# Kernel tuning notes

Measured on AMD Instinct MI355X. Metric: run time of the kernel, lower is better.

## Reference

```python
import jax, jax.numpy as jnp
import numpy as np

N_NODES = 50000
N_EDGES = 800000
N_GRAPHS = 64
IN_DIM, HID1, HID2, N_CLASSES = 128, 256, 128, 10


def setup_inputs() -> dict:
    key = jax.random.key(0)
    ks = jax.random.split(key, 12)
    x = jax.random.normal(ks[0], (N_NODES, IN_DIM), dtype=jnp.float32)
    src = jax.random.randint(ks[1], (N_EDGES,), 0, N_NODES, dtype=jnp.int32)
    dst = jax.random.randint(ks[2], (N_EDGES,), 0, N_NODES, dtype=jnp.int32)
    graph_id = jnp.sort(jax.random.randint(ks[3], (N_NODES,), 0, N_GRAPHS, dtype=jnp.int32))
    s1 = 1.0 / np.sqrt(IN_DIM)
    s2 = 1.0 / np.sqrt(HID1)
    s3 = 1.0 / np.sqrt(HID2)
    s4 = 1.0 / np.sqrt(12)
    return {
        'x': x, 'src': src, 'dst': dst, 'graph_id': graph_id,
        'W1': jax.random.normal(ks[4], (IN_DIM, HID1), dtype=jnp.float32) * s1,
        'b1': jnp.zeros((HID1,), dtype=jnp.float32),
        'W2': jax.random.normal(ks[5], (HID1, HID2), dtype=jnp.float32) * s2,
        'b2': jnp.zeros((HID2,), dtype=jnp.float32),
        'Wc1': jax.random.normal(ks[6], (HID2, 12), dtype=jnp.float32) * s3,
        'bc1': jnp.zeros((12,), dtype=jnp.float32),
        'Wc2': jax.random.normal(ks[7], (12, 12), dtype=jnp.float32) * s4,
        'bc2': jnp.zeros((12,), dtype=jnp.float32),
        'Wc3': jax.random.normal(ks[8], (12, N_CLASSES), dtype=jnp.float32) * s4,
        'bc3': jnp.zeros((N_CLASSES,), dtype=jnp.float32),
    }


def _graph_conv(x, W, b, src, dst, inv_sqrt_out, inv_sqrt_in, n_nodes):
    # DGL GraphConv, norm='both': D_out^{-1/2} applied to source feats,
    # sum-aggregate over edges, then D_in^{-1/2} on destination, then +bias.
    # Weight applied first (equivalent by linearity; reduces gather traffic
    # when out_dim < in_dim, and is exactly what DGL does in that case).
    xw = (x * inv_sqrt_out[:, None]) @ W                      # [N, out]
    agg = jax.ops.segment_sum(xw[src], dst, num_segments=n_nodes)  # SpMM
    return agg * inv_sqrt_in[:, None] + b


def reference(x, src, dst, graph_id, W1, b1, W2, b2, Wc1, bc1, Wc2, bc2, Wc3, bc3):
    n = x.shape[0]
    ones_e = jnp.ones(src.shape, dtype=x.dtype)
    deg_out = jnp.maximum(jax.ops.segment_sum(ones_e, src, num_segments=n), 1.0)
    deg_in = jnp.maximum(jax.ops.segment_sum(ones_e, dst, num_segments=n), 1.0)
    inv_o = jax.lax.rsqrt(deg_out)
    inv_i = jax.lax.rsqrt(deg_in)

    h = jax.nn.relu(_graph_conv(x, W1, b1, src, dst, inv_o, inv_i, n))
    h = jax.nn.relu(_graph_conv(h, W2, b2, src, dst, inv_o, inv_i, n))

    # dgl.mean_nodes: per-graph mean over nodes of the batched graph
    gsum = jax.ops.segment_sum(h, graph_id, num_segments=N_GRAPHS)   # [G, HID2]
    cnt = jnp.maximum(jax.ops.segment_sum(jnp.ones((n,), dtype=h.dtype), graph_id, num_segments=N_GRAPHS), 1.0)
    hg = gsum / cnt[:, None]

    # tiny 3-layer MLP (no activations in between, as in the source)
    out = hg @ Wc1 + bc1
    out = out @ Wc2 + bc2
    out = out @ Wc3 + bc3
    return out
```

## Files before the change

### kernel.cpp

```cpp
#include <hip/hip_runtime.h>
#include <hip/hip_bf16.h>

#define IN_DIM 128
#define HID1 256
#define HID2 128
#define QS_INV (6.0f / 127.0f)
#define QS_FWD (127.0f / 6.0f)

#define HB_BINS 12500
#define HB_WORDS 6250
#define HB_CHUNKS 64
#define BK_SHIFT 8
#define NBUCK 196
#define NCHUNK 256
#define PADCAP 2048

__global__ __launch_bounds__(256) void hist_coarse(const int* __restrict__ src,
                                                   const int* __restrict__ dst, int E,
                                                   int hchunk, int schunk, int nhist,
                                                   int* __restrict__ part, int N,
                                                   int* __restrict__ ccnt,
                                                   float* __restrict__ hg, int hg_n) {
    __shared__ int sm[HB_WORDS];
    __shared__ int cnt[NBUCK];
    const int b = blockIdx.x;
    const int t = threadIdx.x;
    if (b < nhist) {
        const int base = (b >> 6) * HB_BINS;
        const int ebeg = (b & 63) * hchunk;
        const int eend = min(ebeg + hchunk, E);
        for (int w = t; w < HB_WORDS; w += 256) sm[w] = 0;
        __syncthreads();
        for (int e = ebeg + t; e < eend; e += 256) {
            int v = src[e] - base;
            if ((unsigned)v < (unsigned)HB_BINS)
                atomicAdd(&sm[v >> 1], 1 << ((v & 1) * 16));
        }
        __syncthreads();
        const int nb = min(HB_BINS, N - base);
        int* dp = part + (size_t)(b & 63) * N + base;
        for (int w = t; 2 * w < nb; w += 256) {
            int packed = sm[w];
            int bb = 2 * w;
            dp[bb] = packed & 0xffff;
            if (bb + 1 < nb) dp[bb + 1] = (packed >> 16) & 0xffff;
        }
    } else {
        const int cid = b - nhist;
        if (cid == 0)
            for (int i = t; i < hg_n; i += 256) hg[i] = 0.f;
        for (int i = t; i < NBUCK; i += 256) cnt[i] = 0;
        __syncthreads();
        int ebeg = cid * schunk, eend = min(ebeg + schunk, E);
        for (int e = ebeg + t; e < eend; e += 256)
            atomicAdd(&cnt[dst[e] >> BK_SHIFT], 1);
        __syncthreads();
        for (int i = t; i < NBUCK; i += 256) ccnt[cid * NBUCK + i] = cnt[i];
    }
}

__global__ __launch_bounds__(NCHUNK) void coarse_col(const int* __restrict__ ccnt,
                                                     int* __restrict__ coffpre,
                                                     int* __restrict__ ctot) {
    __shared__ int sm[NCHUNK];
    const int b = blockIdx.x, t = threadIdx.x;
    int v = ccnt[t * NBUCK + b];
    sm[t] = v;
    __syncthreads();
#pragma unroll
    for (int off = 1; off < NCHUNK; off <<= 1) {
        int u = (t >= off) ? sm[t - off] : 0;
        __syncthreads();
        sm[t] += u;
        __syncthreads();
    }
    coffpre[t * NBUCK + b] = sm[t] - v;
    if (t == NCHUNK - 1) ctot[b] = sm[t];
}

__device__ __forceinline__ void scan_bbase(const int* __restrict__ ctot, int* sm, int* bbase) {
    const int t = threadIdx.x;
    int v = (t < NBUCK) ? ctot[t] : 0;
    sm[t] = v;
    __syncthreads();
#pragma unroll
    for (int off = 1; off < 256; off <<= 1) {
        int u = (t >= off) ? sm[t - off] : 0;
        __syncthreads();
        sm[t] += u;
        __syncthreads();
    }
    if (t < NBUCK) bbase[t] = sm[t] - v;
    __syncthreads();
}

__global__ __launch_bounds__(256) void scat_cvt(const int* __restrict__ src,
                                                const int* __restrict__ dst, int E,
                                                int schunk,
                                                const int* __restrict__ coffpre,
                                                const int* __restrict__ ctot,
                                                int2* __restrict__ pairs,
                                                const float* __restrict__ x,
                                                const int* __restrict__ part,
                                                float* __restrict__ inv_o,
                                                float* __restrict__ w_arr,
                                                unsigned char* __restrict__ x_q,
                                                __hip_bfloat16* __restrict__ xw2_bf, int N,
                                                int nNodeBlk,
                                                const float* __restrict__ W1,
                                                __hip_bfloat16* __restrict__ W1t,
                                                const float* __restrict__ W2,
                                                __hip_bfloat16* __restrict__ W2t) {
    const int S1 = IN_DIM * HID1;
    const int S2 = HID1 * HID2;
    __shared__ int sm[256];
    __shared__ int bbase[NBUCK];
    __shared__ int lcur[NBUCK];
    const int b = blockIdx.x;
    const int t = threadIdx.x;
    if (b < NCHUNK) {
        scan_bbase(ctot, sm, bbase);
        for (int i = t; i < NBUCK; i += 256)
            lcur[i] = bbase[i] + coffpre[b * NBUCK + i];
        __syncthreads();
        int ebeg = b * schunk, eend = min(ebeg + schunk, E);
        for (int e = ebeg + t; e < eend; e += 256) {
            int d = dst[e];
            int p = atomicAdd(&lcur[d >> BK_SHIFT], 1);
            pairs[p] = make_int2(src[e], d);
        }
    } else if (b < NCHUNK + nNodeBlk) {
        const int n0 = (b - NCHUNK) * 256;
        const int node = n0 + t;
        if (node < N) {
            int d = 0;
#pragma unroll 4
            for (int ch = 0; ch < HB_CHUNKS; ++ch) d += part[(size_t)ch * N + node];
            float iv = rsqrtf((float)max(d, 1));
            inv_o[node] = iv;
            w_arr[node] = iv * QS_INV;
        }
#pragma unroll 4
        for (int k = 0; k < 32; ++k) {
            int li = k * 256 + t;
            int nl = li >> 5;
            if (n0 + nl < N) {
                int i = n0 * 32 + li;
                float4 v = reinterpret_cast<const float4*>(x)[i];
                int c0 = __float2int_rn(fminf(fmaxf(v.x * QS_FWD, -127.f), 127.f));
                int c1 = __float2int_rn(fminf(fmaxf(v.y * QS_FWD, -127.f), 127.f));
                int c2 = __float2int_rn(fminf(fmaxf(v.z * QS_FWD, -127.f), 127.f));
                int c3 = __float2int_rn(fminf(fmaxf(v.w * QS_FWD, -127.f), 127.f));
                unsigned int pk = (unsigned int)(c0 & 0xff) | ((unsigned int)(c1 & 0xff) << 8) |
                                  ((unsigned int)(c2 & 0xff) << 16) | ((unsigned int)(c3 & 0xff) << 24);
                reinterpret_cast<unsigned int*>(x_q)[i] = pk;
            }
        }
    } else if (b < NCHUNK + nNodeBlk + 256) {
        int idx = (b - NCHUNK - nNodeBlk) * 256 + t;
        if (idx < S1) {
            int k = idx / HID1, n = idx - k * HID1;
            W1t[n * IN_DIM + k] = __float2bfloat16(W1[idx]);
        } else if (idx < S1 + S2) {
            int j = idx - S1;
            int k = j / HID2, n = j - k * HID2;
            W2t[n * HID1 + k] = __float2bfloat16(W2[j]);
        }
    } else {
        if (t < 32)
            reinterpret_cast<unsigned int*>(x_q)[(size_t)N * 32 + t] = 0u;
        else if (t < 64)
            reinterpret_cast<ushort4*>(xw2_bf)[(size_t)N * 32 + (t - 32)] = make_ushort4(0, 0, 0, 0);
    }
}

__global__ __launch_bounds__(256) void scat_b(const int2* __restrict__ pairs,
                                              const int* __restrict__ ctot, int N,
                                              const float* __restrict__ w_arr,
                                              int* __restrict__ rowb,
                                              int* __restrict__ rowe,
                                              float* __restrict__ inv_i,
                                              int* __restrict__ csr_src) {
    __shared__ int sm[256];
    __shared__ int bbase[NBUCK];
    __shared__ int cnt[1 << BK_SHIFT];
    __shared__ int cur[1 << BK_SHIFT];
    const int b = blockIdx.x, t = threadIdx.x;
    scan_bbase(ctot, sm, bbase);
    const int segBase = bbase[b];
    const int segEnd = segBase + ctot[b];
    const int pSegBase = ((bbase[b] + 7) & ~7) + b * PADCAP;
    const int nb0 = b << BK_SHIFT;
    const int nbn = min(256, N - nb0);
    cnt[t] = 0;
    __syncthreads();
    for (int j = segBase + t; j < segEnd; j += 256)
        atomicAdd(&cnt[pairs[j].y - nb0], 1);
    __syncthreads();
    int v = cnt[t];
    int pv = (v + 7) & ~7;
    sm[t] = pv;
    __syncthreads();
#pragma unroll
    for (int off = 1; off < 256; off <<= 1) {
        int u = (t >= off) ? sm[t - off] : 0;
        __syncthreads();
        sm[t] += u;
        __syncthreads();
    }
    int pexcl = sm[t] - pv;
    int pbeg = pSegBase + pexcl;
    cur[t] = pbeg;
    if (t < nbn) {
        rowb[nb0 + t] = pbeg;
        rowe[nb0 + t] = pbeg + pv;
        inv_i[nb0 + t] = rsqrtf((float)max(v, 1));
        for (int k = v; k < pv; ++k) csr_src[pbeg + k] = N;
    }
    __syncthreads();
    for (int j = segBase + t; j < segEnd; j += 256) {
        int2 pr = pairs[j];
        int p = atomicAdd(&cur[pr.y - nb0], 1);
        __hip_bfloat16 wb = __float2bfloat16(w_arr[pr.x]);
        csr_src[p] = ((int)(*(unsigned short*)&wb) << 16) | pr.x;
    }
}

__device__ __forceinline__ void gather_row_i8(const unsigned short* __restrict__ xq,
                                              const int* __restrict__ csr,
                                              int beg, int end, int lane,
                                              float& A0, float& A1) {
    float a0 = 0.f, a1 = 0.f;
    int j = beg;
    for (; j + 16 <= end; j += 16) {
        int4 e0 = *reinterpret_cast<const int4*>(csr + j);
        int4 e1 = *reinterpret_cast<const int4*>(csr + j + 4);
        int4 e2 = *reinterpret_cast<const int4*>(csr + j + 8);
        int4 e3 = *reinterpret_cast<const int4*>(csr + j + 12);
        unsigned short q0  = xq[(size_t)(e0.x & 0xffff) * 64 + lane];
        unsigned short q1  = xq[(size_t)(e0.y & 0xffff) * 64 + lane];
        unsigned short q2  = xq[(size_t)(e0.z & 0xffff) * 64 + lane];
        unsigned short q3  = xq[(size_t)(e0.w & 0xffff) * 64 + lane];
        unsigned short q4  = xq[(size_t)(e1.x & 0xffff) * 64 + lane];
        unsigned short q5  = xq[(size_t)(e1.y & 0xffff) * 64 + lane];
        unsigned short q6  = xq[(size_t)(e1.z & 0xffff) * 64 + lane];
        unsigned short q7  = xq[(size_t)(e1.w & 0xffff) * 64 + lane];
        unsigned short q8  = xq[(size_t)(e2.x & 0xffff) * 64 + lane];
        unsigned short q9  = xq[(size_t)(e2.y & 0xffff) * 64 + lane];
        unsigned short q10 = xq[(size_t)(e2.z & 0xffff) * 64 + lane];
        unsigned short q11 = xq[(size_t)(e2.w & 0xffff) * 64 + lane];
        unsigned short q12 = xq[(size_t)(e3.x & 0xffff) * 64 + lane];
        unsigned short q13 = xq[(size_t)(e3.y & 0xffff) * 64 + lane];
        unsigned short q14 = xq[(size_t)(e3.z & 0xffff) * 64 + lane];
        unsigned short q15 = xq[(size_t)(e3.w & 0xffff) * 64 + lane];
#define ACC_I8(ev, qv) { \
        float w = __uint_as_float((unsigned int)(ev) & 0xffff0000u); \
        a0 += w * (float)(int)(signed char)((qv) & 0xff); \
        a1 += w * (float)(int)(signed char)((qv) >> 8); }
        ACC_I8(e0.x, q0)  ACC_I8(e0.y, q1)  ACC_I8(e0.z, q2)  ACC_I8(e0.w, q3)
        ACC_I8(e1.x, q4)  ACC_I8(e1.y, q5)  ACC_I8(e1.z, q6)  ACC_I8(e1.w, q7)
        ACC_I8(e2.x, q8)  ACC_I8(e2.y, q9)  ACC_I8(e2.z, q10) ACC_I8(e2.w, q11)
        ACC_I8(e3.x, q12) ACC_I8(e3.y, q13) ACC_I8(e3.z, q14) ACC_I8(e3.w, q15)
    }
    if (j + 8 <= end) {
        int4 e0 = *reinterpret_cast<const int4*>(csr + j);
        int4 e1 = *reinterpret_cast<const int4*>(csr + j + 4);
        unsigned short q0 = xq[(size_t)(e0.x & 0xffff) * 64 + lane];
        unsigned short q1 = xq[(size_t)(e0.y & 0xffff) * 64 + lane];
        unsigned short q2 = xq[(size_t)(e0.z & 0xffff) * 64 + lane];
        unsigned short q3 = xq[(size_t)(e0.w & 0xffff) * 64 + lane];
        unsigned short q4 = xq[(size_t)(e1.x & 0xffff) * 64 + lane];
        unsigned short q5 = xq[(size_t)(e1.y & 0xffff) * 64 + lane];
        unsigned short q6 = xq[(size_t)(e1.z & 0xffff) * 64 + lane];
        unsigned short q7 = xq[(size_t)(e1.w & 0xffff) * 64 + lane];
        ACC_I8(e0.x, q0) ACC_I8(e0.y, q1) ACC_I8(e0.z, q2) ACC_I8(e0.w, q3)
        ACC_I8(e1.x, q4) ACC_I8(e1.y, q5) ACC_I8(e1.z, q6) ACC_I8(e1.w, q7)
        j += 8;
    }
    for (; j < end; ++j) {
        int ev = csr[j];
        unsigned short qv = xq[(size_t)(ev & 0xffff) * 64 + lane];
        ACC_I8(ev, qv)
    }
#undef ACC_I8
    A0 = a0; A1 = a1;
}

__global__ __launch_bounds__(256) void spmm_kernel(const unsigned short* __restrict__ xq,
                                                   const int* __restrict__ rowb,
                                                   const int* __restrict__ rowe,
                                                   const int* __restrict__ csr_src,
                                                   __hip_bfloat16* __restrict__ out_bf, int N) {
    const int node = blockIdx.x * 4 + (threadIdx.x >> 6);
    if (node >= N) return;
    const int lane = threadIdx.x & 63;
    float a0, a1;
    gather_row_i8(xq, csr_src, rowb[node], rowe[node], lane, a0, a1);
    __hip_bfloat16 b0 = __float2bfloat16(a0);
    __hip_bfloat16 b1 = __float2bfloat16(a1);
    unsigned int packed = (unsigned int)(*(unsigned short*)&b0) |
                          ((unsigned int)(*(unsigned short*)&b1) << 16);
    ((unsigned int*)out_bf)[(size_t)node * 64 + lane] = packed;
}

__device__ __forceinline__ void bf2_unpack(unsigned int p, float& lo, float& hi) {
    lo = __uint_as_float(p << 16);
    hi = __uint_as_float(p & 0xffff0000u);
}

__device__ __forceinline__ void gather_row(const unsigned int* __restrict__ fp,
                                           const int* __restrict__ csr_src,
                                           int beg, int end, int lane,
                                           float& A0, float& A1) {
    float a0 = 0.f, a1 = 0.f;
    int j = beg;
    for (; j + 16 <= end; j += 16) {
        int4 i0 = *reinterpret_cast<const int4*>(csr_src + j);
        int4 i1 = *reinterpret_cast<const int4*>(csr_src + j + 4);
        int4 i2 = *reinterpret_cast<const int4*>(csr_src + j + 8);
        int4 i3 = *reinterpret_cast<const int4*>(csr_src + j + 12);
        unsigned int p0  = fp[(size_t)(i0.x & 0xffff) * 64 + lane];
        unsigned int p1  = fp[(size_t)(i0.y & 0xffff) * 64 + lane];
        unsigned int p2  = fp[(size_t)(i0.z & 0xffff) * 64 + lane];
        unsigned int p3  = fp[(size_t)(i0.w & 0xffff) * 64 + lane];
        unsigned int p4  = fp[(size_t)(i1.x & 0xffff) * 64 + lane];
        unsigned int p5  = fp[(size_t)(i1.y & 0xffff) * 64 + lane];
        unsigned int p6  = fp[(size_t)(i1.z & 0xffff) * 64 + lane];
        unsigned int p7  = fp[(size_t)(i1.w & 0xffff) * 64 + lane];
        unsigned int p8  = fp[(size_t)(i2.x & 0xffff) * 64 + lane];
        unsigned int p9  = fp[(size_t)(i2.y & 0xffff) * 64 + lane];
        unsigned int p10 = fp[(size_t)(i2.z & 0xffff) * 64 + lane];
        unsigned int p11 = fp[(size_t)(i2.w & 0xffff) * 64 + lane];
        unsigned int p12 = fp[(size_t)(i3.x & 0xffff) * 64 + lane];
        unsigned int p13 = fp[(size_t)(i3.y & 0xffff) * 64 + lane];
        unsigned int p14 = fp[(size_t)(i3.z & 0xffff) * 64 + lane];
        unsigned int p15 = fp[(size_t)(i3.w & 0xffff) * 64 + lane];
        float lo, hi;
        bf2_unpack(p0,  lo, hi); a0 += lo; a1 += hi;
        bf2_unpack(p1,  lo, hi); a0 += lo; a1 += hi;
        bf2_unpack(p2,  lo, hi); a0 += lo; a1 += hi;
        bf2_unpack(p3,  lo, hi); a0 += lo; a1 += hi;
        bf2_unpack(p4,  lo, hi); a0 += lo; a1 += hi;
        bf2_unpack(p5,  lo, hi); a0 += lo; a1 += hi;
        bf2_unpack(p6,  lo, hi); a0 += lo; a1 += hi;
        bf2_unpack(p7,  lo, hi); a0 += lo; a1 += hi;
        bf2_unpack(p8,  lo, hi); a0 += lo; a1 += hi;
        bf2_unpack(p9,  lo, hi); a0 += lo; a1 += hi;
        bf2_unpack(p10, lo, hi); a0 += lo; a1 += hi;
        bf2_unpack(p11, lo, hi); a0 += lo; a1 += hi;
        bf2_unpack(p12, lo, hi); a0 += lo; a1 += hi;
        bf2_unpack(p13, lo, hi); a0 += lo; a1 += hi;
        bf2_unpack(p14, lo, hi); a0 += lo; a1 += hi;
        bf2_unpack(p15, lo, hi); a0 += lo; a1 += hi;
    }
    if (j + 8 <= end) {
        int4 i0 = *reinterpret_cast<const int4*>(csr_src + j);
        int4 i1 = *reinterpret_cast<const int4*>(csr_src + j + 4);
        unsigned int p0 = fp[(size_t)(i0.x & 0xffff) * 64 + lane];
        unsigned int p1 = fp[(size_t)(i0.y & 0xffff) * 64 + lane];
        unsigned int p2 = fp[(size_t)(i0.z & 0xffff) * 64 + lane];
        unsigned int p3 = fp[(size_t)(i0.w & 0xffff) * 64 + lane];
        unsigned int p4 = fp[(size_t)(i1.x & 0xffff) * 64 + lane];
        unsigned int p5 = fp[(size_t)(i1.y & 0xffff) * 64 + lane];
        unsigned int p6 = fp[(size_t)(i1.z & 0xffff) * 64 + lane];
        unsigned int p7 = fp[(size_t)(i1.w & 0xffff) * 64 + lane];
        float lo, hi;
        bf2_unpack(p0, lo, hi); a0 += lo; a1 += hi;
        bf2_unpack(p1, lo, hi); a0 += lo; a1 += hi;
        bf2_unpack(p2, lo, hi); a0 += lo; a1 += hi;
        bf2_unpack(p3, lo, hi); a0 += lo; a1 += hi;
        bf2_unpack(p4, lo, hi); a0 += lo; a1 += hi;
        bf2_unpack(p5, lo, hi); a0 += lo; a1 += hi;
        bf2_unpack(p6, lo, hi); a0 += lo; a1 += hi;
        bf2_unpack(p7, lo, hi); a0 += lo; a1 += hi;
        j += 8;
    }
    for (; j < end; ++j) {
        unsigned int p0 = fp[(size_t)(csr_src[j] & 0xffff) * 64 + lane];
        float lo, hi;
        bf2_unpack(p0, lo, hi); a0 += lo; a1 += hi;
    }
    A0 = a0; A1 = a1;
}

#define SP_NODES 8
__global__ __launch_bounds__(256) void spmm_pool_kernel(const __hip_bfloat16* __restrict__ feat,
                                                        const int* __restrict__ rowb,
                                                        const int* __restrict__ rowe,
                                                        const int* __restrict__ csr_src,
                                                        const float* __restrict__ inv_i,
                                                        const float* __restrict__ b2,
                                                        const int* __restrict__ graph_id,
                                                        int N, float* __restrict__ hg_sum) {
    const int wave = blockIdx.x * 4 + (threadIdx.x >> 6);
    const int lane = threadIdx.x & 63;
    const int n0 = wave * SP_NODES;
    if (n0 >= N) return;
    const int n1 = min(n0 + SP_NODES, N);
    const unsigned int* fp = (const unsigned int*)feat;
    const float bias0 = b2[2 * lane];
    const float bias1 = b2[2 * lane + 1];
    int g = graph_id[n0];
    float p0s = 0.f, p1s = 0.f;
    for (int node = n0; node < n1; ++node) {
        int gi = graph_id[node];
        if (gi != g) {
            atomicAdd(&hg_sum[g * HID2 + 2 * lane], p0s);
            atomicAdd(&hg_sum[g * HID2 + 2 * lane + 1], p1s);
            p0s = p1s = 0.f;
            g = gi;
        }
        float a0, a1;
        gather_row(fp, csr_src, rowb[node], rowe[node], lane, a0, a1);
        float ii = inv_i[node];
        p0s += fmaxf(a0 * ii + bias0, 0.f);
        p1s += fmaxf(a1 * ii + bias1, 0.f);
    }
    atomicAdd(&hg_sum[g * HID2 + 2 * lane], p0s);
    atomicAdd(&hg_sum[g * HID2 + 2 * lane + 1], p1s);
}

#define GBM 128
#define GBN 128
#define GBK 32
typedef __attribute__((ext_vector_type(4))) float floatx4;
typedef __attribute__((ext_vector_type(8))) short shortx8;

__device__ __forceinline__ void gload_lds16(const void* g, void* l) {
    __builtin_amdgcn_global_load_lds(
        (const __attribute__((address_space(1))) unsigned int*)g,
        (__attribute__((address_space(3))) unsigned int*)l, 16, 0, 0);
}

__global__ __launch_bounds__(256) void mfma_gemm_kernel(const __hip_bfloat16* __restrict__ A,
                                                        const __hip_bfloat16* __restrict__ Bt,
                                                        __hip_bfloat16* __restrict__ C,
                                                        const float* __restrict__ scaleR,
                                                        const float* __restrict__ bias,
                                                        const float* __restrict__ scaleO,
                                                        int M, int Nn, int K, int doRelu) {
    __shared__ __align__(16) __hip_bfloat16 As[GBM * GBK];
    __shared__ __align__(16) __hip_bfloat16 Bs[GBN * GBK];
    const int tid = threadIdx.x;
    const int bm = blockIdx.x * GBM;
    const int bn = blockIdx.y * GBN;
    const int wid = tid >> 6;
    const int lane = tid & 63;
    const int wm = (wid & 1) * 64;
    const int wn = (wid >> 1) * 64;
    const int lrow = lane & 15;
    const int quad = lane >> 4;

    floatx4 acc[4][4] = {};

    for (int k0 = 0; k0 < K; k0 += GBK) {
#pragma unroll
        for (int c = 0; c < 2; ++c) {
            int slot = c * 256 + tid;
            int r = slot >> 2;
            int ko = (slot & 3) << 3;
            gload_lds16(A + (size_t)(bm + r) * K + k0 + ko,
                        (char*)As + c * 4096 + wid * 1024);
        }
#pragma unroll
        for (int c = 0; c < 2; ++c) {
            int slot = c * 256 + tid;
            int r = slot >> 2;
            int ko = (slot & 3) << 3;
            gload_lds16(Bt + (size_t)(bn + r) * K + k0 + ko,
                        (char*)Bs + c * 4096 + wid * 1024);
        }
        __syncthreads();

        shortx8 af[4], bf[4];
#pragma unroll
        for (int i = 0; i < 4; ++i)
            af[i] = *reinterpret_cast<const shortx8*>(&As[(wm + i * 16 + lrow) * GBK + quad * 8]);
#pragma unroll
        for (int i = 0; i < 4; ++i)
            bf[i] = *reinterpret_cast<const shortx8*>(&Bs[(wn + i * 16 + lrow) * GBK + quad * 8]);
#pragma unroll
        for (int im = 0; im < 4; ++im)
#pragma unroll
            for (int in = 0; in < 4; ++in)
                acc[im][in] = __builtin_amdgcn_mfma_f32_16x16x32_bf16(af[im], bf[in], acc[im][in], 0, 0, 0);
        __syncthreads();
    }

    float bv[4];
#pragma unroll
    for (int in = 0; in < 4; ++in)
        bv[in] = bias ? bias[bn + wn + in * 16 + lrow] : 0.f;

#pragma unroll
    for (int im = 0; im < 4; ++im) {
#pragma unroll
        for (int reg = 0; reg < 4; ++reg) {
            int r = bm + wm + im * 16 + quad * 4 + reg;
            if (r >= M) continue;
            float sR = scaleR ? scaleR[r] : 1.f;
            float sO = scaleO ? scaleO[r] : 1.f;
#pragma unroll
            for (int in = 0; in < 4; ++in) {
                int cc = bn + wn + in * 16 + lrow;
                float v = acc[im][in][reg] * sR + bv[in];
                if (doRelu) v = fmaxf(v, 0.f);
                v *= sO;
                C[(size_t)r * Nn + cc] = __float2bfloat16(v);
            }
        }
    }
}

__device__ __forceinline__ int lower_bound_i(const int* a, int n, int key) {
    int lo = 0, hi = n;
    while (lo < hi) {
        int mid = (lo + hi) >> 1;
        if (a[mid] < key) lo = mid + 1; else hi = mid;
    }
    return lo;
}

__global__ __launch_bounds__(64) void mlp_kernel(const float* __restrict__ hg_sum,
                                                 const int* __restrict__ graph_id, int n,
                                                 const float* __restrict__ Wc1, const float* __restrict__ bc1,
                                                 const float* __restrict__ Wc2, const float* __restrict__ bc2,
                                                 const float* __restrict__ Wc3, const float* __restrict__ bc3,
                                                 float* __restrict__ out) {
    const int g = blockIdx.x;
    const int t = threadIdx.x;
    __shared__ float h[HID2];
    __shared__ float t1[12];
    __shared__ float t2[12];
    __shared__ float s_inv_cnt;
    if (t == 0) {
        int beg = lower_bound_i(graph_id, n, g);
        int end = lower_bound_i(graph_id, n, g + 1);
        int c = end - beg;
        s_inv_cnt = 1.0f / (float)max(c, 1);
    }
    __syncthreads();
    const float ic = s_inv_cnt;
    for (int i = t; i < HID2; i += 64) h[i] = hg_sum[g * HID2 + i] * ic;
    __syncthreads();
    if (t < 12) {
        float a = bc1[t];
        for (int k = 0; k < HID2; ++k) a += h[k] * Wc1[k * 12 + t];
        t1[t] = a;
    }
    __syncthreads();
    if (t < 12) {
        float a = bc2[t];
        for (int k = 0; k < 12; ++k) a += t1[k] * Wc2[k * 12 + t];
        t2[t] = a;
    }
    __syncthreads();
    if (t < 10) {
        float a = bc3[t];
        for (int k = 0; k < 12; ++k) a += t2[k] * Wc3[k * 10 + t];
        out[g * 10 + t] = a;
    }
}

extern "C" void kernel_launch(void* const* d_in, const int* in_sizes, int n_in,
                              void* d_out, int out_size, void* d_ws, size_t ws_size,
                              hipStream_t stream) {
    const float* x        = (const float*)d_in[0];
    const int*   src      = (const int*)d_in[1];
    const int*   dst      = (const int*)d_in[2];
    const int*   graph_id = (const int*)d_in[3];
    const float* W1       = (const float*)d_in[4];
    const float* b1       = (const float*)d_in[5];
    const float* W2       = (const float*)d_in[6];
    const float* b2       = (const float*)d_in[7];
    const float* Wc1      = (const float*)d_in[8];
    const float* bc1      = (const float*)d_in[9];
    const float* Wc2      = (const float*)d_in[10];
    const float* bc2      = (const float*)d_in[11];
    const float* Wc3      = (const float*)d_in[12];
    const float* bc3      = (const float*)d_in[13];
    float* out = (float*)d_out;

    const int N = in_sizes[0] / IN_DIM;
    const int E = in_sizes[1];
    const int G = out_size / 10;

    char* ws = (char*)d_ws;
    size_t off = 0;
    auto alloc = [&](size_t bytes) -> char* {
        char* p = ws + off;
        off = (off + bytes + 255) & ~(size_t)255;
        return p;
    };
    float* inv_i   = (float*)alloc((size_t)N * 4);
    float* inv_o   = (float*)alloc((size_t)N * 4);
    float* w_arr   = (float*)alloc((size_t)N * 4);
    int*   rowb    = (int*)alloc((size_t)N * 4);
    int*   rowe    = (int*)alloc((size_t)N * 4);
    int*   ccnt    = (int*)alloc((size_t)NCHUNK * NBUCK * 4);
    int*   coffpre = (int*)alloc((size_t)NCHUNK * NBUCK * 4);
    int*   ctot    = (int*)alloc((size_t)NBUCK * 4);
    int2*  pairs   = (int2*)alloc((size_t)E * 8);
    int*   csr_src = (int*)alloc(((size_t)E + (size_t)NBUCK * PADCAP + 64) * 4);
    float* hg      = (float*)alloc((size_t)G * HID2 * 4);
    unsigned char* x_q = (unsigned char*)alloc((size_t)(N + 1) * IN_DIM);
    __hip_bfloat16* W1t     = (__hip_bfloat16*)alloc((size_t)IN_DIM * HID1 * 2);
    __hip_bfloat16* W2t     = (__hip_bfloat16*)alloc((size_t)HID1 * HID2 * 2);
    __hip_bfloat16* agg1_bf = (__hip_bfloat16*)alloc((size_t)N * IN_DIM * 2);
    __hip_bfloat16* h1_bf   = (__hip_bfloat16*)alloc((size_t)N * HID1 * 2);
    __hip_bfloat16* xw2_bf  = (__hip_bfloat16*)alloc((size_t)(N + 1) * HID2 * 2);

    int* part = (int*)h1_bf;

    const int hchunk = (E + HB_CHUNKS - 1) / HB_CHUNKS;
    const int n_ranges = (N + HB_BINS - 1) / HB_BINS;
    const int nhist = HB_CHUNKS * n_ranges;
    const int schunk = (E + NCHUNK - 1) / NCHUNK;
    hist_coarse<<<nhist + NCHUNK, 256, 0, stream>>>(src, dst, E, hchunk, schunk, nhist,
                                                    part, N, ccnt, hg, G * HID2);

    coarse_col<<<NBUCK, NCHUNK, 0, stream>>>(ccnt, coffpre, ctot);

    const int nNodeBlk = (N + 255) / 256;
    const int wblk = (IN_DIM * HID1 + HID1 * HID2 + 255) / 256;
    scat_cvt<<<NCHUNK + nNodeBlk + wblk + 1, 256, 0, stream>>>(
        src, dst, E, schunk, coffpre, ctot, pairs,
        x, part, inv_o, w_arr, x_q, xw2_bf, N, nNodeBlk, W1, W1t, W2, W2t);

    scat_b<<<NBUCK, 256, 0, stream>>>(pairs, ctot, N, w_arr, rowb, rowe, inv_i, csr_src);

    spmm_kernel<<<(N + 3) / 4, 256, 0, stream>>>((const unsigned short*)x_q, rowb, rowe,
                                                 csr_src, agg1_bf, N);
    mfma_gemm_kernel<<<dim3((N + GBM - 1) / GBM, HID1 / GBN), 256, 0, stream>>>(
        agg1_bf, W1t, h1_bf, inv_i, b1, inv_o, N, HID1, IN_DIM, 1);

    mfma_gemm_kernel<<<dim3((N + GBM - 1) / GBM, HID2 / GBN), 256, 0, stream>>>(
        h1_bf, W2t, xw2_bf, nullptr, nullptr, nullptr, N, HID2, HID1, 0);
    const int npw = (N + SP_NODES - 1) / SP_NODES;
    spmm_pool_kernel<<<(npw + 3) / 4, 256, 0, stream>>>(xw2_bf, rowb, rowe, csr_src, inv_i, b2,
                                                        graph_id, N, hg);

    mlp_kernel<<<G, 64, 0, stream>>>(hg, graph_id, N, Wc1, bc1, Wc2, bc2, Wc3, bc3, out);
}
```

Before: 255.1 us.

## Quantize layer-2 features to int8 with dynamic absmax before pooled SpMM gather

The second GEMM now computes a global absolute maximum of its bf16 output through a wave reduction and an atomicMax. A new kernel then quantizes xw2 to int8 using that scale, and the fused SpMM+pool kernel gathers 2-byte int8 pairs with integer accumulation instead of 4-byte bf16 pairs, rescaling once per node. This halves the random-gather traffic of the second aggregation. In exchange it adds an extra pass over xw2, an atomic reduction in the GEMM epilogue, and int8 quantization error.

Result: slower. 280.7 us (+10.0%).

```diff
diff --git a/kernel.cpp b/kernel.cpp
--- a/kernel.cpp
+++ b/kernel.cpp
@@ -20,7 +20,8 @@
                                                    int hchunk, int schunk, int nhist,
                                                    int* __restrict__ part, int N,
                                                    int* __restrict__ ccnt,
-                                                   float* __restrict__ hg, int hg_n) {
+                                                   float* __restrict__ hg, int hg_n,
+                                                   float* __restrict__ absm) {
     __shared__ int sm[HB_WORDS];
     __shared__ int cnt[NBUCK];
     const int b = blockIdx.x;
@@ -47,8 +48,10 @@
         }
     } else {
         const int cid = b - nhist;
-        if (cid == 0)
+        if (cid == 0) {
             for (int i = t; i < hg_n; i += 256) hg[i] = 0.f;
+            if (t == 0) *absm = 0.f;
+        }
         for (int i = t; i < NBUCK; i += 256) cnt[i] = 0;
         __syncthreads();
         int ebeg = cid * schunk, eend = min(ebeg + schunk, E);
@@ -303,88 +306,85 @@
     ((unsigned int*)out_bf)[(size_t)node * 64 + lane] = packed;
 }
 
-__device__ __forceinline__ void bf2_unpack(unsigned int p, float& lo, float& hi) {
-    lo = __uint_as_float(p << 16);
-    hi = __uint_as_float(p & 0xffff0000u);
-}
-
-__device__ __forceinline__ void gather_row(const unsigned int* __restrict__ fp,
-                                           const int* __restrict__ csr_src,
-                                           int beg, int end, int lane,
-                                           float& A0, float& A1) {
-    float a0 = 0.f, a1 = 0.f;
+__global__ __launch_bounds__(256) void quant2(const __hip_bfloat16* __restrict__ xw2,
+                                              const float* __restrict__ absm,
+                                              unsigned char* __restrict__ x2q, int n4) {
+    int i = blockIdx.x * 256 + threadIdx.x;
+    if (i >= n4) return;
+    float s = 127.f / fmaxf(*absm, 1e-20f);
+    uint2 v = reinterpret_cast<const uint2*>(xw2)[i];
+    float f0 = __uint_as_float(v.x << 16);
+    float f1 = __uint_as_float(v.x & 0xffff0000u);
+    float f2 = __uint_as_float(v.y << 16);
+    float f3 = __uint_as_float(v.y & 0xffff0000u);
+    int c0 = __float2int_rn(fminf(fmaxf(f0 * s, -127.f), 127.f));
+    int c1 = __float2int_rn(fminf(fmaxf(f1 * s, -127.f), 127.f));
+    int c2 = __float2int_rn(fminf(fmaxf(f2 * s, -127.f), 127.f));
+    int c3 = __float2int_rn(fminf(fmaxf(f3 * s, -127.f), 127.f));
+    unsigned int pk = (unsigned int)(c0 & 0xff) | ((unsigned int)(c1 & 0xff) << 8) |
+                      ((unsigned int)(c2 & 0xff) << 16) | ((unsigned int)(c3 & 0xff) << 24);
+    reinterpret_cast<unsigned int*>(x2q)[i] = pk;
+}
+
+__device__ __forceinline__ void gather_i8_sum(const unsigned short* __restrict__ xq,
+                                              const int* __restrict__ csr,
+                                              int beg, int end, int lane,
+                                              int& A0, int& A1) {
+    int a0 = 0, a1 = 0;
     int j = beg;
     for (; j + 16 <= end; j += 16) {
-        int4 i0 = *reinterpret_cast<const int4*>(csr_src + j);
-        int4 i1 = *reinterpret_cast<const int4*>(csr_src + j + 4);
-        int4 i2 = *reinterpret_cast<const int4*>(csr_src + j + 8);
-        int4 i3 = *reinterpret_cast<const int4*>(csr_src + j + 12);
-        unsigned int p0  = fp[(size_t)(i0.x & 0xffff) * 64 + lane];
-        unsigned int p1  = fp[(size_t)(i0.y & 0xffff) * 64 + lane];
-        unsigned int p2  = fp[(size_t)(i0.z & 0xffff) * 64 + lane];
-        unsigned int p3  = fp[(size_t)(i0.w & 0xffff) * 64 + lane];
-        unsigned int p4  = fp[(size_t)(i1.x & 0xffff) * 64 + lane];
-        unsigned int p5  = fp[(size_t)(i1.y & 0xffff) * 64 + lane];
-        unsigned int p6  = fp[(size_t)(i1.z & 0xffff) * 64 + lane];
-        unsigned int p7  = fp[(size_t)(i1.w & 0xffff) * 64 + lane];
-        unsigned int p8  = fp[(size_t)(i2.x & 0xffff) * 64 + lane];
-        unsigned int p9  = fp[(size_t)(i2.y & 0xffff) * 64 + lane];
-        unsigned int p10 = fp[(size_t)(i2.z & 0xffff) * 64 + lane];
-        unsigned int p11 = fp[(size_t)(i2.w & 0xffff) * 64 + lane];
-        unsigned int p12 = fp[(size_t)(i3.x & 0xffff) * 64 + lane];
-        unsigned int p13 = fp[(size_t)(i3.y & 0xffff) * 64 + lane];
-        unsigned int p14 = fp[(size_t)(i3.z & 0xffff) * 64 + lane];
-        unsigned int p15 = fp[(size_t)(i3.w & 0xffff) * 64 + lane];
-        float lo, hi;
-        bf2_unpack(p0,  lo, hi); a0 += lo; a1 += hi;
-        bf2_unpack(p1,  lo, hi); a0 += lo; a1 += hi;
-        bf2_unpack(p2,  lo, hi); a0 += lo; a1 += hi;
-        bf2_unpack(p3,  lo, hi); a0 += lo; a1 += hi;
-        bf2_unpack(p4,  lo, hi); a0 += lo; a1 += hi;
-        bf2_unpack(p5,  lo, hi); a0 += lo; a1 += hi;
-        bf2_unpack(p6,  lo, hi); a0 += lo; a1 += hi;
-        bf2_unpack(p7,  lo, hi); a0 += lo; a1 += hi;
-        bf2_unpack(p8,  lo, hi); a0 += lo; a1 += hi;
-        bf2_unpack(p9,  lo, hi); a0 += lo; a1 += hi;
-        bf2_unpack(p10, lo, hi); a0 += lo; a1 += hi;
-        bf2_unpack(p11, lo, hi); a0 += lo; a1 += hi;
-        bf2_unpack(p12, lo, hi); a0 += lo; a1 += hi;
-        bf2_unpack(p13, lo, hi); a0 += lo; a1 += hi;
-        bf2_unpack(p14, lo, hi); a0 += lo; a1 += hi;
-        bf2_unpack(p15, lo, hi); a0 += lo; a1 += hi;
+        int4 e0 = *reinterpret_cast<const int4*>(csr + j);
+        int4 e1 = *reinterpret_cast<const int4*>(csr + j + 4);
+        int4 e2 = *reinterpret_cast<const int4*>(csr + j + 8);
+        int4 e3 = *reinterpret_cast<const int4*>(csr + j + 12);
+        unsigned short q0  = xq[(size_t)(e0.x & 0xffff) * 64 + lane];
+        unsigned short q1  = xq[(size_t)(e0.y & 0xffff) * 64 + lane];
+        unsigned short q2  = xq[(size_t)(e0.z & 0xffff) * 64 + lane];
+        unsigned short q3  = xq[(size_t)(e0.w & 0xffff) * 64 + lane];
+        unsigned short q4  = xq[(size_t)(e1.x & 0xffff) * 64 + lane];
+        unsigned short q5  = xq[(size_t)(e1.y & 0xffff) * 64 + lane];
+        unsigned short q6  = xq[(size_t)(e1.z & 0xffff) * 64 + lane];
+        unsigned short q7  = xq[(size_t)(e1.w & 0xffff) * 64 + lane];
+        unsigned short q8  = xq[(size_t)(e2.x & 0xffff) * 64 + lane];
+        unsigned short q9  = xq[(size_t)(e2.y & 0xffff) * 64 + lane];
+        unsigned short q10 = xq[(size_t)(e2.z & 0xffff) * 64 + lane];
+        unsigned short q11 = xq[(size_t)(e2.w & 0xffff) * 64 + lane];
+        unsigned short q12 = xq[(size_t)(e3.x & 0xffff) * 64 + lane];
+        unsigned short q13 = xq[(size_t)(e3.y & 0xffff) * 64 + lane];
+        unsigned short q14 = xq[(size_t)(e3.z & 0xffff) * 64 + lane];
+        unsigned short q15 = xq[(size_t)(e3.w & 0xffff) * 64 + lane];
+#define ACC_S(qv) { a0 += (int)(signed char)((qv) & 0xff); a1 += (int)(signed char)((qv) >> 8); }
+        ACC_S(q0)  ACC_S(q1)  ACC_S(q2)  ACC_S(q3)
+        ACC_S(q4)  ACC_S(q5)  ACC_S(q6)  ACC_S(q7)
+        ACC_S(q8)  ACC_S(q9)  ACC_S(q10) ACC_S(q11)
+        ACC_S(q12) ACC_S(q13) ACC_S(q14) ACC_S(q15)
     }
     if (j + 8 <= end) {
-        int4 i0 = *reinterpret_cast<const int4*>(csr_src + j);
-        int4 i1 = *reinterpret_cast<const int4*>(csr_src + j + 4);
-        unsigned int p0 = fp[(size_t)(i0.x & 0xffff) * 64 + lane];
-        unsigned int p1 = fp[(size_t)(i0.y & 0xffff) * 64 + lane];
-        unsigned int p2 = fp[(size_t)(i0.z & 0xffff) * 64 + lane];
-        unsigned int p3 = fp[(size_t)(i0.w & 0xffff) * 64 + lane];
-        unsigned int p4 = fp[(size_t)(i1.x & 0xffff) * 64 + lane];
-        unsigned int p5 = fp[(size_t)(i1.y & 0xffff) * 64 + lane];
-        unsigned int p6 = fp[(size_t)(i1.z & 0xffff) * 64 + lane];
-        unsigned int p7 = fp[(size_t)(i1.w & 0xffff) * 64 + lane];
-        float lo, hi;
-        bf2_unpack(p0, lo, hi); a0 += lo; a1 += hi;
-        bf2_unpack(p1, lo, hi); a0 += lo; a1 += hi;
-        bf2_unpack(p2, lo, hi); a0 += lo; a1 += hi;
-        bf2_unpack(p3, lo, hi); a0 += lo; a1 += hi;
-        bf2_unpack(p4, lo, hi); a0 += lo; a1 += hi;
-        bf2_unpack(p5, lo, hi); a0 += lo; a1 += hi;
-        bf2_unpack(p6, lo, hi); a0 += lo; a1 += hi;
-        bf2_unpack(p7, lo, hi); a0 += lo; a1 += hi;
+        int4 e0 = *reinterpret_cast<const int4*>(csr + j);
+        int4 e1 = *reinterpret_cast<const int4*>(csr + j + 4);
+        unsigned short q0 = xq[(size_t)(e0.x & 0xffff) * 64 + lane];
+        unsigned short q1 = xq[(size_t)(e0.y & 0xffff) * 64 + lane];
+        unsigned short q2 = xq[(size_t)(e0.z & 0xffff) * 64 + lane];
+        unsigned short q3 = xq[(size_t)(e0.w & 0xffff) * 64 + lane];
+        unsigned short q4 = xq[(size_t)(e1.x & 0xffff) * 64 + lane];
+        unsigned short q5 = xq[(size_t)(e1.y & 0xffff) * 64 + lane];
+        unsigned short q6 = xq[(size_t)(e1.z & 0xffff) * 64 + lane];
+        unsigned short q7 = xq[(size_t)(e1.w & 0xffff) * 64 + lane];
+        ACC_S(q0) ACC_S(q1) ACC_S(q2) ACC_S(q3)
+        ACC_S(q4) ACC_S(q5) ACC_S(q6) ACC_S(q7)
         j += 8;
     }
     for (; j < end; ++j) {
-        unsigned int p0 = fp[(size_t)(csr_src[j] & 0xffff) * 64 + lane];
-        float lo, hi;
-        bf2_unpack(p0, lo, hi); a0 += lo; a1 += hi;
-    }
+        unsigned short qv = xq[(size_t)(csr[j] & 0xffff) * 64 + lane];
+        ACC_S(qv)
+    }
+#undef ACC_S
     A0 = a0; A1 = a1;
 }
 
 #define SP_NODES 8
-__global__ __launch_bounds__(256) void spmm_pool_kernel(const __hip_bfloat16* __restrict__ feat,
+__global__ __launch_bounds__(256) void spmm_pool_kernel(const unsigned short* __restrict__ x2q,
+                                                        const float* __restrict__ absm,
                                                         const int* __restrict__ rowb,
                                                         const int* __restrict__ rowe,
                                                         const int* __restrict__ csr_src,
@@ -397,7 +397,7 @@
     const int n0 = wave * SP_NODES;
     if (n0 >= N) return;
     const int n1 = min(n0 + SP_NODES, N);
-    const unsigned int* fp = (const unsigned int*)feat;
+    const float step = fmaxf(*absm, 1e-20f) * (1.0f / 127.0f);
     const float bias0 = b2[2 * lane];
     const float bias1 = b2[2 * lane + 1];
     int g = graph_id[n0];
@@ -410,11 +410,11 @@
             p0s = p1s = 0.f;
             g = gi;
         }
-        float a0, a1;
-        gather_row(fp, csr_src, rowb[node], rowe[node], lane, a0, a1);
-        float ii = inv_i[node];
-        p0s += fmaxf(a0 * ii + bias0, 0.f);
-        p1s += fmaxf(a1 * ii + bias1, 0.f);
+        int a0i, a1i;
+        gather_i8_sum(x2q, csr_src, rowb[node], rowe[node], lane, a0i, a1i);
+        float iis = inv_i[node] * step;
+        p0s += fmaxf((float)a0i * iis + bias0, 0.f);
+        p1s += fmaxf((float)a1i * iis + bias1, 0.f);
     }
     atomicAdd(&hg_sum[g * HID2 + 2 * lane], p0s);
     atomicAdd(&hg_sum[g * HID2 + 2 * lane + 1], p1s);
@@ -438,6 +438,7 @@
                                                         const float* __restrict__ scaleR,
                                                         const float* __restrict__ bias,
                                                         const float* __restrict__ scaleO,
+                                                        float* __restrict__ absmax_out,
                                                         int M, int Nn, int K, int doRelu) {
     __shared__ __align__(16) __hip_bfloat16 As[GBM * GBK];
     __shared__ __align__(16) __hip_bfloat16 Bs[GBN * GBK];
@@ -492,6 +493,7 @@
     for (int in = 0; in < 4; ++in)
         bv[in] = bias ? bias[bn + wn + in * 16 + lrow] : 0.f;
 
+    float mloc = 0.f;
 #pragma unroll
     for (int im = 0; im < 4; ++im) {
 #pragma unroll
@@ -506,9 +508,17 @@
                 float v = acc[im][in][reg] * sR + bv[in];
                 if (doRelu) v = fmaxf(v, 0.f);
                 v *= sO;
+                mloc = fmaxf(mloc, fabsf(v));
                 C[(size_t)r * Nn + cc] = __float2bfloat16(v);
             }
         }
+    }
+    if (absmax_out) {
+#pragma unroll
+        for (int off = 1; off < 64; off <<= 1)
+            mloc = fmaxf(mloc, __shfl_xor(mloc, off));
+        if (lane == 0)
+            atomicMax((unsigned int*)absmax_out, __float_as_uint(mloc));
     }
 }
 
@@ -595,6 +605,7 @@
     float* inv_i   = (float*)alloc((size_t)N * 4);
     float* inv_o   = (float*)alloc((size_t)N * 4);
     float* w_arr   = (float*)alloc((size_t)N * 4);
+    float* absm    = (float*)alloc(4);
     int*   rowb    = (int*)alloc((size_t)N * 4);
     int*   rowe    = (int*)alloc((size_t)N * 4);
     int*   ccnt    = (int*)alloc((size_t)NCHUNK * NBUCK * 4);
@@ -603,7 +614,8 @@
     int2*  pairs   = (int2*)alloc((size_t)E * 8);
     int*   csr_src = (int*)alloc(((size_t)E + (size_t)NBUCK * PADCAP + 64) * 4);
     float* hg      = (float*)alloc((size_t)G * HID2 * 4);
-    unsigned char* x_q = (unsigned char*)alloc((size_t)(N + 1) * IN_DIM);
+    unsigned char* x_q  = (unsigned char*)alloc((size_t)(N + 1) * IN_DIM);
+    unsigned char* x2q  = (unsigned char*)alloc((size_t)(N + 1) * HID2);
     __hip_bfloat16* W1t     = (__hip_bfloat16*)alloc((size_t)IN_DIM * HID1 * 2);
     __hip_bfloat16* W2t     = (__hip_bfloat16*)alloc((size_t)HID1 * HID2 * 2);
     __hip_bfloat16* agg1_bf = (__hip_bfloat16*)alloc((size_t)N * IN_DIM * 2);
@@ -617,7 +629,7 @@
     const int nhist = HB_CHUNKS * n_ranges;
     const int schunk = (E + NCHUNK - 1) / NCHUNK;
     hist_coarse<<<nhist + NCHUNK, 256, 0, stream>>>(src, dst, E, hchunk, schunk, nhist,
-                                                    part, N, ccnt, hg, G * HID2);
+                                                    part, N, ccnt, hg, G * HID2, absm);
 
     coarse_col<<<NBUCK, NCHUNK, 0, stream>>>(ccnt, coffpre, ctot);
 
@@ -632,12 +644,15 @@
     spmm_kernel<<<(N + 3) / 4, 256, 0, stream>>>((const unsigned short*)x_q, rowb, rowe,
                                                  csr_src, agg1_bf, N);
     mfma_gemm_kernel<<<dim3((N + GBM - 1) / GBM, HID1 / GBN), 256, 0, stream>>>(
-        agg1_bf, W1t, h1_bf, inv_i, b1, inv_o, N, HID1, IN_DIM, 1);
+        agg1_bf, W1t, h1_bf, inv_i, b1, inv_o, nullptr, N, HID1, IN_DIM, 1);
 
     mfma_gemm_kernel<<<dim3((N + GBM - 1) / GBM, HID2 / GBN), 256, 0, stream>>>(
-        h1_bf, W2t, xw2_bf, nullptr, nullptr, nullptr, N, HID2, HID1, 0);
+        h1_bf, W2t, xw2_bf, nullptr, nullptr, nullptr, absm, N, HID2, HID1, 0);
+    const int n4q = (N + 1) * HID2 / 4;
+    quant2<<<(n4q + 255) / 256, 256, 0, stream>>>(xw2_bf, absm, x2q, n4q);
     const int npw = (N + SP_NODES - 1) / SP_NODES;
-    spmm_pool_kernel<<<(npw + 3) / 4, 256, 0, stream>>>(xw2_bf, rowb, rowe, csr_src, inv_i, b2,
+    spmm_pool_kernel<<<(npw + 3) / 4, 256, 0, stream>>>((const unsigned short*)x2q, absm,
+                                                        rowb, rowe, csr_src, inv_i, b2,
                                                         graph_id, N, hg);
 
     mlp_kernel<<<G, 64, 0, stream>>>(hg, graph_id, N, Wc1, bc1, Wc2, bc2, Wc3, bc3, out);
```
